# Performance work log

Hardware: AMD Instinct MI355X
Metric: run time of the kernel (lower is better)

Reference implementation:

```python
import jax, jax.numpy as jnp
import numpy as np

B, T, N = 8, 20, 256
BN = B * N
IN_DIM, H, HEADS, DH = 2, 128, 8, 16
FF = 4 * H
LAYERS = 5
EPS = 1e-5


def _ln(h, g, b):
    mu = h.mean(-1, keepdims=True)
    v = ((h - mu) ** 2).mean(-1, keepdims=True)
    return (h - mu) * jax.lax.rsqrt(v + EPS) * g + b


def setup_inputs() -> dict:
    key = jax.random.key(0)
    ks = jax.random.split(key, 16)
    ego_mask = jax.random.uniform(ks[0], (B, T, N)) > 0.2
    ego_mask = ego_mask.at[:, 0, :].set(True)  # every node active at t=0 (no fully-padded sequence)
    x_raw = jax.random.normal(ks[1], (T, BN, IN_DIM), dtype=jnp.float32)
    adj = (jax.random.uniform(ks[2], (T, BN, BN)) < 0.01).astype(jnp.float32)
    s = 0.02
    p = {}
    p['gcn1_w'] = jax.random.normal(ks[3], (IN_DIM, H), jnp.float32) * s
    p['gcn_ws'] = jax.random.normal(ks[4], (5, H, H), jnp.float32) * s
    p['gcn_bs'] = jnp.zeros((6, H), jnp.float32)
    p['ln_g'] = jnp.ones((6, H), jnp.float32)
    p['ln_b'] = jnp.zeros((6, H), jnp.float32)
    p['pos_embed'] = jax.random.normal(ks[5], (T, H), jnp.float32) * s
    p['t_wqkv'] = jax.random.normal(ks[6], (LAYERS, 3 * H, H), jnp.float32) * s
    p['t_bqkv'] = jnp.zeros((LAYERS, 3 * H), jnp.float32)
    p['t_wo'] = jax.random.normal(ks[7], (LAYERS, H, H), jnp.float32) * s
    p['t_bo'] = jnp.zeros((LAYERS, H), jnp.float32)
    p['t_ln1g'] = jnp.ones((LAYERS, H), jnp.float32)
    p['t_ln1b'] = jnp.zeros((LAYERS, H), jnp.float32)
    p['t_w1'] = jax.random.normal(ks[8], (LAYERS, FF, H), jnp.float32) * s
    p['t_b1'] = jnp.zeros((LAYERS, FF), jnp.float32)
    p['t_w2'] = jax.random.normal(ks[9], (LAYERS, H, FF), jnp.float32) * s
    p['t_b2'] = jnp.zeros((LAYERS, H), jnp.float32)
    p['t_ln2g'] = jnp.ones((LAYERS, H), jnp.float32)
    p['t_ln2b'] = jnp.zeros((LAYERS, H), jnp.float32)
    return dict(ego_mask=ego_mask, x_raw=x_raw, adj=adj, **p)


def _forward(ego_mask, x_raw, adj, gcn1_w, gcn_ws, gcn_bs, ln_g, ln_b, pos_embed,
             t_wqkv, t_bqkv, t_wo, t_bo, t_ln1g, t_ln1b, t_w1, t_b1, t_w2, t_b2,
             t_ln2g, t_ln2b):
    mask_flat = ego_mask.transpose(1, 0, 2).reshape(T, BN).astype(x_raw.dtype)  # [T, BN]

    def per_t(x_t, A_t, m):
        # masked subgraph + self-loops only on active nodes (PyG GCNConv on x[idx], A[idx][:,idx])
        Am = A_t * m[:, None] * m[None, :]
        Ahat = Am + jnp.diag(m)
        deg = Ahat.sum(0)                       # gcn_norm: degree at target (col of edge_index)
        dinv = jnp.where(deg > 0, jax.lax.rsqrt(deg), 0.0)
        S = (dinv[:, None] * Ahat * dinv[None, :]).T  # out[dst] = sum_src norm * x[src]

        def gcn(h, W, b):
            return S @ (h @ W) + b

        h = jax.nn.relu(_ln(gcn(x_t, gcn1_w, gcn_bs[0]), ln_g[0], ln_b[0]))
        for i in range(5):
            hr = _ln(gcn(h, gcn_ws[i], gcn_bs[i + 1]), ln_g[i + 1], ln_b[i + 1])
            h = jax.nn.relu(hr + h)  # residual then ReLU, as in source
        return h * m[:, None]        # inactive rows stay zero (x_placeholder)

    x_ph = jax.vmap(per_t)(x_raw, adj, mask_flat)          # [T, BN, H]
    x = x_ph.transpose(1, 0, 2) + pos_embed[None]          # [BN, T, H]

    # src_key_padding_mask: True = padded -> -inf on keys
    key_bias = jnp.where(mask_flat.T.astype(bool), 0.0, -jnp.inf)[:, None, None, :]  # [BN,1,1,T]
    scale = 1.0 / np.sqrt(DH)
    for l in range(LAYERS):  # post-norm TransformerEncoderLayer, activation=relu, eval (no dropout)
        qkv = x @ t_wqkv[l].T + t_bqkv[l]
        q, k, v = jnp.split(qkv, 3, axis=-1)
        q = q.reshape(BN, T, HEADS, DH)
        k = k.reshape(BN, T, HEADS, DH)
        v = v.reshape(BN, T, HEADS, DH)
        sc = jnp.einsum('bqhd,bkhd->bhqk', q, k) * scale + key_bias
        a = jax.nn.softmax(sc, axis=-1)
        o = jnp.einsum('bhqk,bkhd->bqhd', a, v).reshape(BN, T, H)
        o = o @ t_wo[l].T + t_bo[l]
        x = _ln(x + o, t_ln1g[l], t_ln1b[l])
        ff = jax.nn.relu(x @ t_w1[l].T + t_b1[l]) @ t_w2[l].T + t_b2[l]
        x = _ln(x + ff, t_ln2g[l], t_ln2b[l])
    return x.reshape(B, N, T, H)


def reference(ego_mask, x_raw, adj, gcn1_w, gcn_ws, gcn_bs, ln_g, ln_b, pos_embed,
              t_wqkv, t_bqkv, t_wo, t_bo, t_ln1g, t_ln1b, t_w1, t_b1, t_w2, t_b2,
              t_ln2g, t_ln2b):
    return _forward(ego_mask, x_raw, adj, gcn1_w, gcn_ws, gcn_bs, ln_g, ln_b,
                    pos_embed, t_wqkv, t_bqkv, t_wo, t_bo, t_ln1g, t_ln1b,
                    t_w1, t_b1, t_w2, t_b2, t_ln2g, t_ln2b)
```

## Files before the change

kernel.cpp:

```cpp
#include <hip/hip_runtime.h>
#include <hip/hip_bf16.h>
#include <cstdint>
#include <cstddef>

#define BNODES 2048
#define NT 20
#define HDIM 128
#define NROWS (NT * BNODES)
#define CAP 64
#define QP 129

typedef __attribute__((ext_vector_type(8))) short short8;
typedef __attribute__((ext_vector_type(4))) float floatx4;

__device__ __forceinline__ float bf2f(short u) {
  return __uint_as_float(((unsigned int)(unsigned short)u) << 16);
}
__device__ __forceinline__ unsigned int pack2(float a, float b) {
  __hip_bfloat16 b0 = __float2bfloat16(a), b1 = __float2bfloat16(b);
  return ((unsigned int)*(unsigned short*)&b1 << 16) | *(unsigned short*)&b0;
}

__global__ void setup_kernel(const void* __restrict__ ego, float* __restrict__ maskf,
                             int* __restrict__ colcnt,
                             const float* __restrict__ twqkv, const float* __restrict__ two,
                             const float* __restrict__ tw1, const float* __restrict__ tw2,
                             const float* __restrict__ gcnws,
                             __hip_bfloat16* __restrict__ wqkv, __hip_bfloat16* __restrict__ wo,
                             __hip_bfloat16* __restrict__ w1, __hip_bfloat16* __restrict__ w2,
                             __hip_bfloat16* __restrict__ wsT) {
  int gid = blockIdx.x * blockDim.x + threadIdx.x;
  if (gid < NROWS) {
    unsigned int w0 = ((const unsigned int*)ego)[0];
    int val;
    if (w0 == 1u)                 val = ((const int*)ego)[gid] != 0;
    else if (w0 == 0x3F800000u)   val = ((const float*)ego)[gid] != 0.0f;
    else if (w0 == 0x3F803F80u)   val = ((const unsigned short*)ego)[gid] != 0;
    else                          val = ((const unsigned char*)ego)[gid] != 0;
    int b = gid / (NT * 256);
    int t = (gid / 256) % NT;
    int n = gid % 256;
    maskf[t * BNODES + b * 256 + n] = val ? 1.0f : 0.0f;
    colcnt[gid] = 0;
    return;
  }
  gid -= NROWS;
  if (gid < 245760) { wqkv[gid] = __float2bfloat16(twqkv[gid]); return; }
  gid -= 245760;
  if (gid < 81920) { wo[gid] = __float2bfloat16(two[gid]); return; }
  gid -= 81920;
  if (gid < 327680) { w1[gid] = __float2bfloat16(tw1[gid]); return; }
  gid -= 327680;
  if (gid < 327680) { w2[gid] = __float2bfloat16(tw2[gid]); return; }
  gid -= 327680;
  if (gid < 81920) {
    int l = gid >> 14, rem = gid & 16383;
    int n = rem >> 7, k = rem & 127;
    wsT[gid] = __float2bfloat16(gcnws[(l << 14) + (k << 7) + n]);
  }
}

__global__ __launch_bounds__(256) void build_edges_kernel(const float* __restrict__ adj,
                                                          const float* __restrict__ maskf,
                                                          int* __restrict__ colcnt,
                                                          int* __restrict__ colidx) {
  size_t e4 = (size_t)blockIdx.x * 256 + threadIdx.x;
  size_t e = e4 * 4;
  size_t row = e >> 11;
  if (maskf[row] == 0.0f) return;
  const float4 a = ((const float4*)adj)[e4];
  if (a.x == 0.0f && a.y == 0.0f && a.z == 0.0f && a.w == 0.0f) return;
  int i0 = (int)(e & (BNODES - 1));
  int t = (int)(row >> 11);
  int j = (int)(row & (BNODES - 1));
  int base = t * BNODES;
  if (a.x != 0.0f) { int p = atomicAdd(&colcnt[base + i0 + 0], 1); if (p < CAP) colidx[(size_t)(base + i0 + 0) * CAP + p] = j; }
  if (a.y != 0.0f) { int p = atomicAdd(&colcnt[base + i0 + 1], 1); if (p < CAP) colidx[(size_t)(base + i0 + 1) * CAP + p] = j; }
  if (a.z != 0.0f) { int p = atomicAdd(&colcnt[base + i0 + 2], 1); if (p < CAP) colidx[(size_t)(base + i0 + 2) * CAP + p] = j; }
  if (a.w != 0.0f) { int p = atomicAdd(&colcnt[base + i0 + 3], 1); if (p < CAP) colidx[(size_t)(base + i0 + 3) * CAP + p] = j; }
}

__global__ void finalize_deg_kernel(const float* __restrict__ maskf, int* __restrict__ colcnt,
                                    float* __restrict__ dinv) {
  int gid = blockIdx.x * blockDim.x + threadIdx.x;
  if (gid >= NROWS) return;
  int cnt = colcnt[gid];
  dinv[gid] = (maskf[gid] != 0.0f) ? rsqrtf((float)cnt + 1.0f) : 0.0f;
  colcnt[gid] = cnt < CAP ? cnt : CAP;
}

__global__ __launch_bounds__(256) void spmm_ln0_kernel(const float* __restrict__ xraw,
                                                       const float* __restrict__ gw,
                                                       const float* __restrict__ dinv,
                                                       const int* __restrict__ colcnt,
                                                       const int* __restrict__ colidx,
                                                       const float* __restrict__ bias,
                                                       const float* __restrict__ gamma,
                                                       const float* __restrict__ beta,
                                                       float* __restrict__ dstF,
                                                       __hip_bfloat16* __restrict__ dstB) {
  int tid = threadIdx.x;
  int r = (blockIdx.x << 2) + (tid >> 6);
  int lane = tid & 63;
  int c0 = lane << 1;
  int t = r >> 11;
  float di = dinv[r];
  float g00 = gw[c0], g01 = gw[c0 + 1], g10 = gw[HDIM + c0], g11 = gw[HDIM + c0 + 1];
  float a0 = 0.0f, a1 = 0.0f;
  if (di != 0.0f) {
    float x0 = xraw[2 * r], x1 = xraw[2 * r + 1];
    a0 = di * fmaf(x0, g00, x1 * g10);
    a1 = di * fmaf(x0, g01, x1 * g11);
    int cnt = colcnt[r];
    const int* cols = colidx + (size_t)r * CAP;
    const float* dt = dinv + (t << 11);
    for (int k = 0; k < cnt; ++k) {
      int j = cols[k];
      size_t gr = ((size_t)t << 11) + j;
      float y0 = xraw[2 * gr], y1 = xraw[2 * gr + 1];
      float dj = dt[j];
      a0 = fmaf(dj, fmaf(y0, g00, y1 * g10), a0);
      a1 = fmaf(dj, fmaf(y0, g01, y1 * g11), a1);
    }
    a0 *= di; a1 *= di;
  }
  a0 += bias[c0]; a1 += bias[c0 + 1];
  float s = a0 + a1, q = a0 * a0 + a1 * a1;
  #pragma unroll
  for (int off = 32; off > 0; off >>= 1) {
    s += __shfl_xor(s, off, 64);
    q += __shfl_xor(q, off, 64);
  }
  float mu = s * (1.0f / HDIM);
  float var = fmaxf(q * (1.0f / HDIM) - mu * mu, 0.0f);
  float rs = rsqrtf(var + 1e-5f);
  float o0 = fmaxf((a0 - mu) * rs * gamma[c0] + beta[c0], 0.0f);
  float o1 = fmaxf((a1 - mu) * rs * gamma[c0 + 1] + beta[c0 + 1], 0.0f);
  size_t oi = (size_t)r * HDIM + c0;
  *(float2*)(dstF + oi) = make_float2(o0, o1);
  *(unsigned int*)((char*)dstB + oi * 2) = pack2(o0, o1);
}

__global__ __launch_bounds__(256) void spmm_kernel(const __hip_bfloat16* __restrict__ Y,
                                                   const float* __restrict__ dinv,
                                                   const int* __restrict__ colcnt,
                                                   const int* __restrict__ colidx,
                                                   __hip_bfloat16* __restrict__ out) {
  int tid = threadIdx.x;
  int r = (blockIdx.x << 2) + (tid >> 6);
  int lane = tid & 63;
  int t = r >> 11;
  float di = dinv[r];
  const unsigned int* Yrow = (const unsigned int*)((const short*)Y + (size_t)r * HDIM) + lane;
  unsigned int* orow = (unsigned int*)((short*)out + (size_t)r * HDIM) + lane;
  if (di == 0.0f) { *orow = 0u; return; }
  unsigned int sv = *Yrow;
  float a0 = di * bf2f((short)(sv & 0xffff));
  float a1 = di * bf2f((short)(sv >> 16));
  int cnt = colcnt[r];
  const int* cols = colidx + (size_t)r * CAP;
  const float* dt = dinv + (t << 11);
  const unsigned int* Yt = (const unsigned int*)((const short*)Y + (((size_t)t << 11) * HDIM)) + lane;
  for (int k = 0; k < cnt; ++k) {
    int j = cols[k];
    float dj = dt[j];
    unsigned int v = Yt[(size_t)j << 6];
    a0 = fmaf(dj, bf2f((short)(v & 0xffff)), a0);
    a1 = fmaf(dj, bf2f((short)(v >> 16)), a1);
  }
  a0 *= di; a1 *= di;
  *orow = pack2(a0, a1);
}

__device__ __forceinline__ void async16(const void* g, void* l) {
  __builtin_amdgcn_global_load_lds(
      (const __attribute__((address_space(1))) unsigned int*)g,
      (__attribute__((address_space(3))) unsigned int*)l, 16, 0, 0);
}

__global__ __launch_bounds__(256) void gemm_plain(const __hip_bfloat16* __restrict__ A,
                                                  const __hip_bfloat16* __restrict__ Bt,
                                                  const float* __restrict__ bias,
                                                  int K, int N, int relu,
                                                  __hip_bfloat16* __restrict__ Cb) {
  __shared__ __align__(16) char smem[65536];
  __hip_bfloat16* As = (__hip_bfloat16*)smem;
  __hip_bfloat16* Bs = As + 128 * 128;
  const int tid = threadIdx.x;
  const int wv = tid >> 6, ln = tid & 63;
  const int n0 = blockIdx.x << 7, m0 = blockIdx.y << 7;
  const int wm = (wv & 1) << 6, wn = (wv >> 1) << 6;
  const int lr = ln & 15, lq = ln >> 4;

  floatx4 acc[4][4];
  #pragma unroll
  for (int mi = 0; mi < 4; ++mi)
    #pragma unroll
    for (int ni = 0; ni < 4; ++ni) acc[mi][ni] = (floatx4)0.0f;

  for (int k0 = 0; k0 < K; k0 += 128) {
    if (k0) __syncthreads();
    #pragma unroll
    for (int i = 0; i < 8; ++i) {
      int rloc = i * 16 + wv * 4 + lq;
      int sc = (ln & 15) ^ (rloc & 15);
      async16((const char*)A + ((size_t)(m0 + rloc) * K + k0) * 2 + (size_t)sc * 16,
              (char*)As + (size_t)(i * 16 + wv * 4) * 256);
      async16((const char*)Bt + ((size_t)(n0 + rloc) * K + k0) * 2 + (size_t)sc * 16,
              (char*)Bs + (size_t)(i * 16 + wv * 4) * 256);
    }
    __syncthreads();
    #pragma unroll
    for (int kc = 0; kc < 4; ++kc) {
      short8 af[4], bfr[4];
      #pragma unroll
      for (int mi = 0; mi < 4; ++mi) {
        int R = wm + (mi << 4) + lr;
        int ch = ((kc << 2) + lq) ^ (R & 15);
        af[mi] = *(const short8*)(As + (R << 7) + (ch << 3));
      }
      #pragma unroll
      for (int ni = 0; ni < 4; ++ni) {
        int R = wn + (ni << 4) + lr;
        int ch = ((kc << 2) + lq) ^ (R & 15);
        bfr[ni] = *(const short8*)(Bs + (R << 7) + (ch << 3));
      }
      #pragma unroll
      for (int mi = 0; mi < 4; ++mi)
        #pragma unroll
        for (int ni = 0; ni < 4; ++ni)
          acc[mi][ni] = __builtin_amdgcn_mfma_f32_16x16x32_bf16(af[mi], bfr[ni], acc[mi][ni], 0, 0, 0);
    }
  }
  #pragma unroll
  for (int ni = 0; ni < 4; ++ni) {
    int cn = n0 + wn + (ni << 4) + lr;
    float bv = bias ? bias[cn] : 0.0f;
    #pragma unroll
    for (int mi = 0; mi < 4; ++mi) {
      #pragma unroll
      for (int r = 0; r < 4; ++r) {
        int rm = m0 + wm + (mi << 4) + (lq << 2) + r;
        float v = acc[mi][ni][r] + bv;
        if (relu) v = fmaxf(v, 0.0f);
        Cb[(size_t)rm * N + cn] = __float2bfloat16(v);
      }
    }
  }
}

__global__ __launch_bounds__(256) void gemm_ln(const __hip_bfloat16* __restrict__ A,
                                               const __hip_bfloat16* __restrict__ Bt,
                                               const float* __restrict__ bias,
                                               int K, int gcn_mode,
                                               const float* __restrict__ residF,
                                               const float* __restrict__ lng,
                                               const float* __restrict__ lnb,
                                               const float* __restrict__ maskf,
                                               const float* __restrict__ pos,
                                               float* __restrict__ outF,
                                               __hip_bfloat16* __restrict__ outB) {
  __shared__ __align__(16) char smem[49152];
  __hip_bfloat16* As = (__hip_bfloat16*)smem;
  __hip_bfloat16* Bs = As + 64 * 128;
  float* Cs = (float*)smem;
  const int tid = threadIdx.x;
  const int wv = tid >> 6, ln = tid & 63;
  const int m0 = blockIdx.x << 6;
  const int wm = (wv & 1) << 5, wn = (wv >> 1) << 6;
  const int lr = ln & 15, lq = ln >> 4;

  floatx4 acc[2][4];
  #pragma unroll
  for (int mi = 0; mi < 2; ++mi)
    #pragma unroll
    for (int ni = 0; ni < 4; ++ni) acc[mi][ni] = (floatx4)0.0f;

  for (int k0 = 0; k0 < K; k0 += 128) {
    if (k0) __syncthreads();
    #pragma unroll
    for (int i = 0; i < 4; ++i) {
      int rloc = i * 16 + wv * 4 + lq;
      int sc = (ln & 15) ^ (rloc & 15);
      async16((const char*)A + ((size_t)(m0 + rloc) * K + k0) * 2 + (size_t)sc * 16,
              (char*)As + (size_t)(i * 16 + wv * 4) * 256);
    }
    #pragma unroll
    for (int i = 0; i < 8; ++i) {
      int rloc = i * 16 + wv * 4 + lq;
      int sc = (ln & 15) ^ (rloc & 15);
      async16((const char*)Bt + ((size_t)rloc * K + k0) * 2 + (size_t)sc * 16,
              (char*)Bs + (size_t)(i * 16 + wv * 4) * 256);
    }
    __syncthreads();
    #pragma unroll
    for (int kc = 0; kc < 4; ++kc) {
      short8 af[2], bfr[4];
      #pragma unroll
      for (int mi = 0; mi < 2; ++mi) {
        int R = wm + (mi << 4) + lr;
        int ch = ((kc << 2) + lq) ^ (R & 15);
        af[mi] = *(const short8*)(As + (R << 7) + (ch << 3));
      }
      #pragma unroll
      for (int ni = 0; ni < 4; ++ni) {
        int R = wn + (ni << 4) + lr;
        int ch = ((kc << 2) + lq) ^ (R & 15);
        bfr[ni] = *(const short8*)(Bs + (R << 7) + (ch << 3));
      }
      #pragma unroll
      for (int mi = 0; mi < 2; ++mi)
        #pragma unroll
        for (int ni = 0; ni < 4; ++ni)
          acc[mi][ni] = __builtin_amdgcn_mfma_f32_16x16x32_bf16(af[mi], bfr[ni], acc[mi][ni], 0, 0, 0);
    }
  }

  __syncthreads();
  #pragma unroll
  for (int ni = 0; ni < 4; ++ni) {
    int cn = wn + (ni << 4) + lr;
    float bv = bias[cn];
    #pragma unroll
    for (int mi = 0; mi < 2; ++mi) {
      #pragma unroll
      for (int r = 0; r < 4; ++r) {
        int rl = wm + (mi << 4) + (lq << 2) + r;
        float v = acc[mi][ni][r] + bv;
        if (!gcn_mode) v += residF[(size_t)(m0 + rl) * HDIM + cn];
        Cs[(rl << 7) + cn] = v;
      }
    }
  }
  __syncthreads();
  float2 gam = *(const float2*)(lng + ln * 2);
  float2 bet = *(const float2*)(lnb + ln * 2);
  #pragma unroll 4
  for (int p = 0; p < 16; ++p) {
    int rl = p * 4 + wv;
    int grow = m0 + rl;
    float2 xv = *(const float2*)(Cs + (rl << 7) + ln * 2);
    float s = xv.x + xv.y, q = xv.x * xv.x + xv.y * xv.y;
    #pragma unroll
    for (int off = 32; off > 0; off >>= 1) {
      s += __shfl_xor(s, off, 64);
      q += __shfl_xor(q, off, 64);
    }
    float mu = s * (1.0f / HDIM);
    float var = fmaxf(q * (1.0f / HDIM) - mu * mu, 0.0f);
    float rs = rsqrtf(var + 1e-5f);
    float o0 = (xv.x - mu) * rs * gam.x + bet.x;
    float o1 = (xv.y - mu) * rs * gam.y + bet.y;
    if (gcn_mode) {
      float2 rv = *(const float2*)(residF + (size_t)grow * HDIM + ln * 2);
      o0 = fmaxf(o0 + rv.x, 0.0f);
      o1 = fmaxf(o1 + rv.y, 0.0f);
    }
    size_t oi;
    if (pos) {
      int t = grow >> 11, bn = grow & (BNODES - 1);
      float m = maskf[grow];
      float2 pv = *(const float2*)(pos + t * HDIM + ln * 2);
      o0 = o0 * m + pv.x;
      o1 = o1 * m + pv.y;
      oi = ((size_t)bn * NT + t) * HDIM + ln * 2;
    } else {
      oi = (size_t)grow * HDIM + ln * 2;
    }
    if (outF) *(float2*)(outF + oi) = make_float2(o0, o1);
    if (outB) *(unsigned int*)((char*)outB + oi * 2) = pack2(o0, o1);
  }
}

__global__ __launch_bounds__(256) void attn_kernel(const __hip_bfloat16* __restrict__ qkv,
                                                   const float* __restrict__ maskf,
                                                   __hip_bfloat16* __restrict__ o) {
  int bn = blockIdx.x;
  __shared__ float q[NT][QP], kk[NT][QP], vv[NT][QP];
  __shared__ float mb[NT];
  int tid = threadIdx.x;
  if (tid < NT) mb[tid] = (maskf[tid * BNODES + bn] == 0.0f) ? -1e30f : 0.0f;
  for (int idx = tid; idx < NT * 48; idx += 256) {
    int t = idx / 48, c8 = idx % 48;
    short8 v8 = *(const short8*)((const short*)qkv + ((size_t)bn * NT + t) * 384 + c8 * 8);
    float* dst = (c8 < 16) ? &q[t][c8 * 8] : (c8 < 32) ? &kk[t][(c8 - 16) * 8] : &vv[t][(c8 - 32) * 8];
    #pragma unroll
    for (int i = 0; i < 8; ++i) dst[i] = bf2f(v8[i]);
  }
  __syncthreads();
  if (tid >= 8 * NT) return;
  int h = tid / NT, tq = tid % NT;
  float qr[16];
  #pragma unroll
  for (int d = 0; d < 16; ++d) qr[d] = q[tq][h * 16 + d];
  float p[NT];
  float mx = -1e30f;
  #pragma unroll
  for (int tk = 0; tk < NT; ++tk) {
    float s = 0.0f;
    #pragma unroll
    for (int d = 0; d < 16; ++d) s = fmaf(qr[d], kk[tk][h * 16 + d], s);
    s = s * 0.25f + mb[tk];
    p[tk] = s;
    mx = fmaxf(mx, s);
  }
  float sum = 0.0f;
  #pragma unroll
  for (int tk = 0; tk < NT; ++tk) { float e = __expf(p[tk] - mx); p[tk] = e; sum += e; }
  float inv = 1.0f / sum;
  float oacc[16];
  #pragma unroll
  for (int d = 0; d < 16; ++d) oacc[d] = 0.0f;
  #pragma unroll
  for (int tk = 0; tk < NT; ++tk) {
    float pv = p[tk] * inv;
    #pragma unroll
    for (int d = 0; d < 16; ++d) oacc[d] = fmaf(pv, vv[tk][h * 16 + d], oacc[d]);
  }
  short* op = (short*)o + ((size_t)bn * NT + tq) * HDIM + h * 16;
  short8 o8a, o8b;
  #pragma unroll
  for (int d = 0; d < 8; ++d) {
    __hip_bfloat16 b = __float2bfloat16(oacc[d]);
    o8a[d] = *(short*)&b;
  }
  #pragma unroll
  for (int d = 0; d < 8; ++d) {
    __hip_bfloat16 b = __float2bfloat16(oacc[8 + d]);
    o8b[d] = *(short*)&b;
  }
  *(short8*)op = o8a;
  *(short8*)(op + 8) = o8b;
}

extern "C" void kernel_launch(void* const* d_in, const int* in_sizes, int n_in,
                              void* d_out, int out_size, void* d_ws, size_t ws_size,
                              hipStream_t stream) {
  const void*  ego   = d_in[0];
  const float* xraw  = (const float*)d_in[1];
  const float* adj   = (const float*)d_in[2];
  const float* gcn1w = (const float*)d_in[3];
  const float* gcnws = (const float*)d_in[4];
  const float* gcnbs = (const float*)d_in[5];
  const float* lng   = (const float*)d_in[6];
  const float* lnb   = (const float*)d_in[7];
  const float* pos   = (const float*)d_in[8];
  const float* twqkv = (const float*)d_in[9];
  const float* tbqkv = (const float*)d_in[10];
  const float* two   = (const float*)d_in[11];
  const float* tbo   = (const float*)d_in[12];
  const float* tln1g = (const float*)d_in[13];
  const float* tln1b = (const float*)d_in[14];
  const float* tw1   = (const float*)d_in[15];
  const float* tb1   = (const float*)d_in[16];
  const float* tw2   = (const float*)d_in[17];
  const float* tb2   = (const float*)d_in[18];
  const float* tln2g = (const float*)d_in[19];
  const float* tln2b = (const float*)d_in[20];

  char* base = (char*)d_ws;
  size_t off = 0;
  auto alloc = [&](size_t bytes) -> void* {
    void* p = base + off;
    off = (off + bytes + 255) & ~(size_t)255;
    return p;
  };
  float* maskf  = (float*)alloc((size_t)NROWS * 4);
  float* dinv   = (float*)alloc((size_t)NROWS * 4);
  int*   colcnt = (int*)  alloc((size_t)NROWS * 4);
  void*  regA   = alloc((size_t)NROWS * 384 * 2);
  int*   colidx = (int*)regA;
  __hip_bfloat16* qkv_bf = (__hip_bfloat16*)regA;
  void*  regB   = alloc((size_t)NROWS * 512 * 2);
  __hip_bfloat16* g_bf   = (__hip_bfloat16*)regB;
  __hip_bfloat16* big_bf = (__hip_bfloat16*)regB;
  __hip_bfloat16* attn_bf = (__hip_bfloat16*)alloc((size_t)NROWS * HDIM * 2);
  __hip_bfloat16* hbufA   = (__hip_bfloat16*)alloc((size_t)NROWS * HDIM * 2);
  __hip_bfloat16* xbf     = (__hip_bfloat16*)alloc((size_t)NROWS * HDIM * 2);
  float* hbufF  = (float*)alloc((size_t)NROWS * HDIM * 4);
  float* xbuf   = (float*)alloc((size_t)NROWS * HDIM * 4);
  __hip_bfloat16* wqkv_bf = (__hip_bfloat16*)alloc((size_t)245760 * 2);
  __hip_bfloat16* wo_bf   = (__hip_bfloat16*)alloc((size_t)81920 * 2);
  __hip_bfloat16* w1_bf   = (__hip_bfloat16*)alloc((size_t)327680 * 2);
  __hip_bfloat16* w2_bf   = (__hip_bfloat16*)alloc((size_t)327680 * 2);
  __hip_bfloat16* wsT_bf  = (__hip_bfloat16*)alloc((size_t)81920 * 2);

  setup_kernel<<<4320, 256, 0, stream>>>(ego, maskf, colcnt, twqkv, two, tw1, tw2, gcnws,
                                         wqkv_bf, wo_bf, w1_bf, w2_bf, wsT_bf);
  build_edges_kernel<<<81920, 256, 0, stream>>>(adj, maskf, colcnt, colidx);
  finalize_deg_kernel<<<160, 256, 0, stream>>>(maskf, colcnt, dinv);

  spmm_ln0_kernel<<<NROWS / 4, 256, 0, stream>>>(xraw, gcn1w, dinv, colcnt, colidx,
                                                 gcnbs, lng, lnb, hbufF, hbufA);
  for (int i = 0; i < 5; ++i) {
    spmm_kernel<<<NROWS / 4, 256, 0, stream>>>(hbufA, dinv, colcnt, colidx, g_bf);
    const float* fm = (i == 4) ? maskf : nullptr;
    const float* fp = (i == 4) ? pos : nullptr;
    float* oF = (i == 4) ? xbuf : hbufF;
    __hip_bfloat16* oB = (i == 4) ? xbf : hbufA;
    gemm_ln<<<NROWS / 64, 256, 0, stream>>>(
        g_bf, wsT_bf + (size_t)i * 16384, gcnbs + (i + 1) * 128, 128, 1,
        hbufF, lng + (i + 1) * 128, lnb + (i + 1) * 128, fm, fp, oF, oB);
  }

  for (int l = 0; l < 5; ++l) {
    gemm_plain<<<dim3(3, NROWS / 128), 256, 0, stream>>>(
        xbf, wqkv_bf + (size_t)l * 49152, tbqkv + l * 384, 128, 384, 0, qkv_bf);
    attn_kernel<<<BNODES, 256, 0, stream>>>(qkv_bf, maskf, attn_bf);
    gemm_ln<<<NROWS / 64, 256, 0, stream>>>(
        attn_bf, wo_bf + (size_t)l * 16384, tbo + l * 128, 128, 0,
        xbuf, tln1g + l * 128, tln1b + l * 128, nullptr, nullptr, xbuf, xbf);
    gemm_plain<<<dim3(4, NROWS / 128), 256, 0, stream>>>(
        xbf, w1_bf + (size_t)l * 65536, tb1 + l * 512, 128, 512, 1, big_bf);
    float* oF = (l == 4) ? (float*)d_out : xbuf;
    __hip_bfloat16* oB = (l == 4) ? nullptr : xbf;
    gemm_ln<<<NROWS / 64, 256, 0, stream>>>(
        big_bf, w2_bf + (size_t)l * 65536, tb2 + l * 128, 512, 0,
        xbuf, tln2g + l * 128, tln2b + l * 128, nullptr, nullptr, oF, oB);
  }
}
```

Baseline: 1.495 ms.

## Fuse FFN up/down projections with LayerNorm and grid-stride edge building

Adds an ffn_kernel that computes relu(X·W1+b1) into shared memory in 128-column panels and immediately multiplies by W2, then applies bias, residual and LayerNorm. This removes the 512-wide bf16 hidden activation round trip through global memory and one launch per layer. Each block handles 32 rows, so W1 and W2 are re-read for every row block, and the 72KB of shared memory limits occupancy. The edge-building kernel also becomes a grid-stride loop launched with 4096 blocks instead of 81920.

Result: faster. 1.463 ms (median of 2 runs) (-2.2%).

```diff
diff --git a/kernel.cpp b/kernel.cpp
--- a/kernel.cpp
+++ b/kernel.cpp
@@ -19,6 +19,10 @@
 __device__ __forceinline__ unsigned int pack2(float a, float b) {
   __hip_bfloat16 b0 = __float2bfloat16(a), b1 = __float2bfloat16(b);
   return ((unsigned int)*(unsigned short*)&b1 << 16) | *(unsigned short*)&b0;
+}
+__device__ __forceinline__ short f2bf_s(float a) {
+  __hip_bfloat16 b = __float2bfloat16(a);
+  return *(short*)&b;
 }
 
 __global__ void setup_kernel(const void* __restrict__ ego, float* __restrict__ maskf,
@@ -64,20 +68,23 @@
                                                           const float* __restrict__ maskf,
                                                           int* __restrict__ colcnt,
                                                           int* __restrict__ colidx) {
-  size_t e4 = (size_t)blockIdx.x * 256 + threadIdx.x;
-  size_t e = e4 * 4;
-  size_t row = e >> 11;
-  if (maskf[row] == 0.0f) return;
-  const float4 a = ((const float4*)adj)[e4];
-  if (a.x == 0.0f && a.y == 0.0f && a.z == 0.0f && a.w == 0.0f) return;
-  int i0 = (int)(e & (BNODES - 1));
-  int t = (int)(row >> 11);
-  int j = (int)(row & (BNODES - 1));
-  int base = t * BNODES;
-  if (a.x != 0.0f) { int p = atomicAdd(&colcnt[base + i0 + 0], 1); if (p < CAP) colidx[(size_t)(base + i0 + 0) * CAP + p] = j; }
-  if (a.y != 0.0f) { int p = atomicAdd(&colcnt[base + i0 + 1], 1); if (p < CAP) colidx[(size_t)(base + i0 + 1) * CAP + p] = j; }
-  if (a.z != 0.0f) { int p = atomicAdd(&colcnt[base + i0 + 2], 1); if (p < CAP) colidx[(size_t)(base + i0 + 2) * CAP + p] = j; }
-  if (a.w != 0.0f) { int p = atomicAdd(&colcnt[base + i0 + 3], 1); if (p < CAP) colidx[(size_t)(base + i0 + 3) * CAP + p] = j; }
+  const size_t total = (size_t)NROWS * BNODES / 4;
+  const size_t stride = (size_t)gridDim.x * 256;
+  for (size_t e4 = (size_t)blockIdx.x * 256 + threadIdx.x; e4 < total; e4 += stride) {
+    size_t e = e4 * 4;
+    size_t row = e >> 11;
+    if (maskf[row] == 0.0f) continue;
+    const float4 a = ((const float4*)adj)[e4];
+    if (a.x == 0.0f && a.y == 0.0f && a.z == 0.0f && a.w == 0.0f) continue;
+    int i0 = (int)(e & (BNODES - 1));
+    int t = (int)(row >> 11);
+    int j = (int)(row & (BNODES - 1));
+    int base = t * BNODES;
+    if (a.x != 0.0f) { int p = atomicAdd(&colcnt[base + i0 + 0], 1); if (p < CAP) colidx[(size_t)(base + i0 + 0) * CAP + p] = j; }
+    if (a.y != 0.0f) { int p = atomicAdd(&colcnt[base + i0 + 1], 1); if (p < CAP) colidx[(size_t)(base + i0 + 1) * CAP + p] = j; }
+    if (a.z != 0.0f) { int p = atomicAdd(&colcnt[base + i0 + 2], 1); if (p < CAP) colidx[(size_t)(base + i0 + 2) * CAP + p] = j; }
+    if (a.w != 0.0f) { int p = atomicAdd(&colcnt[base + i0 + 3], 1); if (p < CAP) colidx[(size_t)(base + i0 + 3) * CAP + p] = j; }
+  }
 }
 
 __global__ void finalize_deg_kernel(const float* __restrict__ maskf, int* __restrict__ colcnt,
@@ -372,6 +379,168 @@
   }
 }
 
+__global__ __launch_bounds__(256) void ffn_kernel(const __hip_bfloat16* __restrict__ X,
+                                                  const __hip_bfloat16* __restrict__ W1t,
+                                                  const __hip_bfloat16* __restrict__ W2t,
+                                                  const float* __restrict__ b1,
+                                                  const float* __restrict__ b2,
+                                                  const float* __restrict__ residF,
+                                                  const float* __restrict__ lng,
+                                                  const float* __restrict__ lnb,
+                                                  float* __restrict__ outF,
+                                                  __hip_bfloat16* __restrict__ outB) {
+  __shared__ __align__(16) char smem[73728];
+  __hip_bfloat16* As  = (__hip_bfloat16*)smem;
+  __hip_bfloat16* Bs  = (__hip_bfloat16*)(smem + 8192);
+  __hip_bfloat16* Hid = (__hip_bfloat16*)(smem + 40960);
+  float* Cs = (float*)smem;
+  const int tid = threadIdx.x;
+  const int wv = tid >> 6, ln = tid & 63;
+  const int m0 = blockIdx.x << 5;
+  const int wn = wv << 5;
+  const int lr = ln & 15, lq = ln >> 4;
+
+  #pragma unroll
+  for (int i = 0; i < 2; ++i) {
+    int rloc = (i << 4) + (wv << 2) + lq;
+    int sc = (ln & 15) ^ (rloc & 15);
+    async16((const char*)X + ((size_t)(m0 + rloc) * HDIM) * 2 + (size_t)sc * 16,
+            (char*)As + (size_t)((i << 4) + (wv << 2)) * 256);
+  }
+
+  floatx4 acc2[2][2];
+  #pragma unroll
+  for (int mi = 0; mi < 2; ++mi)
+    #pragma unroll
+    for (int ni = 0; ni < 2; ++ni) acc2[mi][ni] = (floatx4)0.0f;
+
+  for (int nc = 0; nc < 4; ++nc) {
+    if (nc) __syncthreads();
+    #pragma unroll
+    for (int i = 0; i < 8; ++i) {
+      int rloc = (i << 4) + (wv << 2) + lq;
+      int sc = (ln & 15) ^ (rloc & 15);
+      async16((const char*)W1t + ((size_t)((nc << 7) + rloc) * HDIM) * 2 + (size_t)sc * 16,
+              (char*)Bs + (size_t)((i << 4) + (wv << 2)) * 256);
+    }
+    __syncthreads();
+    floatx4 acc[2][2];
+    #pragma unroll
+    for (int mi = 0; mi < 2; ++mi)
+      #pragma unroll
+      for (int ni = 0; ni < 2; ++ni) acc[mi][ni] = (floatx4)0.0f;
+    #pragma unroll
+    for (int kc = 0; kc < 4; ++kc) {
+      short8 af[2], bfr[2];
+      #pragma unroll
+      for (int mi = 0; mi < 2; ++mi) {
+        int R = (mi << 4) + lr;
+        int ch = ((kc << 2) + lq) ^ (R & 15);
+        af[mi] = *(const short8*)(As + (R << 7) + (ch << 3));
+      }
+      #pragma unroll
+      for (int ni = 0; ni < 2; ++ni) {
+        int R = wn + (ni << 4) + lr;
+        int ch = ((kc << 2) + lq) ^ (R & 15);
+        bfr[ni] = *(const short8*)(Bs + (R << 7) + (ch << 3));
+      }
+      #pragma unroll
+      for (int mi = 0; mi < 2; ++mi)
+        #pragma unroll
+        for (int ni = 0; ni < 2; ++ni)
+          acc[mi][ni] = __builtin_amdgcn_mfma_f32_16x16x32_bf16(af[mi], bfr[ni], acc[mi][ni], 0, 0, 0);
+    }
+    __hip_bfloat16* panel = Hid + (nc << 12);
+    #pragma unroll
+    for (int ni = 0; ni < 2; ++ni) {
+      int cn = wn + (ni << 4) + lr;
+      float bv = b1[(nc << 7) + cn];
+      #pragma unroll
+      for (int mi = 0; mi < 2; ++mi) {
+        #pragma unroll
+        for (int r = 0; r < 4; ++r) {
+          int row = (mi << 4) + (lq << 2) + r;
+          float v = fmaxf(acc[mi][ni][r] + bv, 0.0f);
+          panel[(row << 7) + ((((cn >> 3) ^ (row & 15)) << 3) | (cn & 7))] = __float2bfloat16(v);
+        }
+      }
+    }
+  }
+  __syncthreads();
+
+  for (int kc2 = 0; kc2 < 4; ++kc2) {
+    if (kc2) __syncthreads();
+    #pragma unroll
+    for (int i = 0; i < 8; ++i) {
+      int rloc = (i << 4) + (wv << 2) + lq;
+      int sc = (ln & 15) ^ (rloc & 15);
+      async16((const char*)W2t + ((size_t)rloc * 512 + (kc2 << 7)) * 2 + (size_t)sc * 16,
+              (char*)Bs + (size_t)((i << 4) + (wv << 2)) * 256);
+    }
+    __syncthreads();
+    const __hip_bfloat16* panel = Hid + (kc2 << 12);
+    #pragma unroll
+    for (int kc = 0; kc < 4; ++kc) {
+      short8 af[2], bfr[2];
+      #pragma unroll
+      for (int mi = 0; mi < 2; ++mi) {
+        int R = (mi << 4) + lr;
+        int ch = ((kc << 2) + lq) ^ (R & 15);
+        af[mi] = *(const short8*)(panel + (R << 7) + (ch << 3));
+      }
+      #pragma unroll
+      for (int ni = 0; ni < 2; ++ni) {
+        int R = wn + (ni << 4) + lr;
+        int ch = ((kc << 2) + lq) ^ (R & 15);
+        bfr[ni] = *(const short8*)(Bs + (R << 7) + (ch << 3));
+      }
+      #pragma unroll
+      for (int mi = 0; mi < 2; ++mi)
+        #pragma unroll
+        for (int ni = 0; ni < 2; ++ni)
+          acc2[mi][ni] = __builtin_amdgcn_mfma_f32_16x16x32_bf16(af[mi], bfr[ni], acc2[mi][ni], 0, 0, 0);
+    }
+  }
+
+  __syncthreads();
+  #pragma unroll
+  for (int ni = 0; ni < 2; ++ni) {
+    int cn = wn + (ni << 4) + lr;
+    float bv = b2[cn];
+    #pragma unroll
+    for (int mi = 0; mi < 2; ++mi) {
+      #pragma unroll
+      for (int r = 0; r < 4; ++r) {
+        int rl = (mi << 4) + (lq << 2) + r;
+        Cs[(rl << 7) + cn] = acc2[mi][ni][r] + bv + residF[(size_t)(m0 + rl) * HDIM + cn];
+      }
+    }
+  }
+  __syncthreads();
+  float2 gam = *(const float2*)(lng + ln * 2);
+  float2 bet = *(const float2*)(lnb + ln * 2);
+  #pragma unroll
+  for (int p = 0; p < 8; ++p) {
+    int rl = (p << 2) + wv;
+    int grow = m0 + rl;
+    float2 xv = *(const float2*)(Cs + (rl << 7) + ln * 2);
+    float s = xv.x + xv.y, q = xv.x * xv.x + xv.y * xv.y;
+    #pragma unroll
+    for (int off = 32; off > 0; off >>= 1) {
+      s += __shfl_xor(s, off, 64);
+      q += __shfl_xor(q, off, 64);
+    }
+    float mu = s * (1.0f / HDIM);
+    float var = fmaxf(q * (1.0f / HDIM) - mu * mu, 0.0f);
+    float rs = rsqrtf(var + 1e-5f);
+    float o0 = (xv.x - mu) * rs * gam.x + bet.x;
+    float o1 = (xv.y - mu) * rs * gam.y + bet.y;
+    size_t oi = (size_t)grow * HDIM + ln * 2;
+    if (outF) *(float2*)(outF + oi) = make_float2(o0, o1);
+    if (outB) *(unsigned int*)((char*)outB + oi * 2) = pack2(o0, o1);
+  }
+}
+
 __global__ __launch_bounds__(256) void attn_kernel(const __hip_bfloat16* __restrict__ qkv,
                                                    const float* __restrict__ maskf,
                                                    __hip_bfloat16* __restrict__ o) {
@@ -420,15 +589,9 @@
   short* op = (short*)o + ((size_t)bn * NT + tq) * HDIM + h * 16;
   short8 o8a, o8b;
   #pragma unroll
-  for (int d = 0; d < 8; ++d) {
-    __hip_bfloat16 b = __float2bfloat16(oacc[d]);
-    o8a[d] = *(short*)&b;
-  }
-  #pragma unroll
-  for (int d = 0; d < 8; ++d) {
-    __hip_bfloat16 b = __float2bfloat16(oacc[8 + d]);
-    o8b[d] = *(short*)&b;
-  }
+  for (int d = 0; d < 8; ++d) o8a[d] = f2bf_s(oacc[d]);
+  #pragma unroll
+  for (int d = 0; d < 8; ++d) o8b[d] = f2bf_s(oacc[8 + d]);
   *(short8*)op = o8a;
   *(short8*)(op + 8) = o8b;
 }
@@ -471,9 +634,7 @@
   void*  regA   = alloc((size_t)NROWS * 384 * 2);
   int*   colidx = (int*)regA;
   __hip_bfloat16* qkv_bf = (__hip_bfloat16*)regA;
-  void*  regB   = alloc((size_t)NROWS * 512 * 2);
-  __hip_bfloat16* g_bf   = (__hip_bfloat16*)regB;
-  __hip_bfloat16* big_bf = (__hip_bfloat16*)regB;
+  __hip_bfloat16* g_bf    = (__hip_bfloat16*)alloc((size_t)NROWS * HDIM * 2);
   __hip_bfloat16* attn_bf = (__hip_bfloat16*)alloc((size_t)NROWS * HDIM * 2);
   __hip_bfloat16* hbufA   = (__hip_bfloat16*)alloc((size_t)NROWS * HDIM * 2);
   __hip_bfloat16* xbf     = (__hip_bfloat16*)alloc((size_t)NROWS * HDIM * 2);
@@ -487,7 +648,7 @@
 
   setup_kernel<<<4320, 256, 0, stream>>>(ego, maskf, colcnt, twqkv, two, tw1, tw2, gcnws,
                                          wqkv_bf, wo_bf, w1_bf, w2_bf, wsT_bf);
-  build_edges_kernel<<<81920, 256, 0, stream>>>(adj, maskf, colcnt, colidx);
+  build_edges_kernel<<<4096, 256, 0, stream>>>(adj, maskf, colcnt, colidx);
   finalize_deg_kernel<<<160, 256, 0, stream>>>(maskf, colcnt, dinv);
 
   spmm_ln0_kernel<<<NROWS / 4, 256, 0, stream>>>(xraw, gcn1w, dinv, colcnt, colidx,
@@ -510,12 +671,11 @@
     gemm_ln<<<NROWS / 64, 256, 0, stream>>>(
         attn_bf, wo_bf + (size_t)l * 16384, tbo + l * 128, 128, 0,
         xbuf, tln1g + l * 128, tln1b + l * 128, nullptr, nullptr, xbuf, xbf);
-    gemm_plain<<<dim3(4, NROWS / 128), 256, 0, stream>>>(
-        xbf, w1_bf + (size_t)l * 65536, tb1 + l * 512, 128, 512, 1, big_bf);
     float* oF = (l == 4) ? (float*)d_out : xbuf;
     __hip_bfloat16* oB = (l == 4) ? nullptr : xbf;
-    gemm_ln<<<NROWS / 64, 256, 0, stream>>>(
-        big_bf, w2_bf + (size_t)l * 65536, tb2 + l * 128, 512, 0,
-        xbuf, tln2g + l * 128, tln2b + l * 128, nullptr, nullptr, oF, oB);
-  }
-}
+    ffn_kernel<<<NROWS / 32, 256, 0, stream>>>(
+        xbf, w1_bf + (size_t)l * 65536, w2_bf + (size_t)l * 65536,
+        tb1 + l * 512, tb2 + l * 128, xbuf,
+        tln2g + l * 128, tln2b + l * 128, oF, oB);
+  }
+}
```
